# Kernel tuning notes

Measured on AMD Instinct MI355X. Metric: run time of the kernel, lower is better.

Reference implementation:

```python
import jax, jax.numpy as jnp
import numpy as np

D_MODEL = 1024
NUM_HEADS = 16
HEAD_DIM = D_MODEL // NUM_HEADS  # 64
# NOTE: the torch module passes scale=attention_head_size (NOT 1/sqrt(dh));
# we reproduce that exact math: scores are MULTIPLIED by head_dim.
SCALE = float(HEAD_DIM)

B, S = 2, 2048


def setup_inputs() -> dict:
    key = jax.random.key(0)
    ks = jax.random.split(key, 6)
    q = jax.random.normal(ks[0], (B, S, D_MODEL), dtype=jnp.float32)
    k = jax.random.normal(ks[1], (B, S, D_MODEL), dtype=jnp.float32)
    v = jax.random.normal(ks[2], (B, S, D_MODEL), dtype=jnp.float32)
    # Linear weights stored as [in, out]; scaled like typical init so the
    # (head_dim-scaled) logits stay numerically sane.
    w_std = 0.02
    Wq = jax.random.normal(ks[3], (D_MODEL, D_MODEL), dtype=jnp.float32) * w_std
    Wk = jax.random.normal(ks[4], (D_MODEL, D_MODEL), dtype=jnp.float32) * w_std
    Wv = jax.random.normal(ks[5], (D_MODEL, D_MODEL), dtype=jnp.float32) * w_std
    return {"q": q, "k": k, "v": v, "Wq": Wq, "Wk": Wk, "Wv": Wv}


def reference(q, k, v, Wq, Wk, Wv):
    Bq, Sq, _ = q.shape
    # QKV projections (qkv_bias=False), split into heads: [B, S, H, dh]
    qh = (q @ Wq).reshape(Bq, Sq, NUM_HEADS, HEAD_DIM)
    kh = (k @ Wk).reshape(Bq, Sq, NUM_HEADS, HEAD_DIM)
    vh = (v @ Wv).reshape(Bq, Sq, NUM_HEADS, HEAD_DIM)
    # Full materialized scores [B, H, Sq, Sk] -- the naive MHA pattern.
    sims = jnp.einsum("bqhd,bkhd->bhqk", qh, kh) * SCALE
    attn = jax.nn.softmax(sims, axis=-1)
    # Second matmul, then merge heads back: [B, S, D]
    out = jnp.einsum("bhqk,bkhd->bqhd", attn, vh).reshape(Bq, Sq, D_MODEL)
    return out
```

## Files before the change

kernel.cpp:

```cpp
#include <hip/hip_runtime.h>
#include <cstdint>
#include <cstddef>

typedef unsigned short u16;
typedef __bf16 bf16x8 __attribute__((ext_vector_type(8)));
typedef float f32x4 __attribute__((ext_vector_type(4)));
typedef unsigned int u32x4 __attribute__((ext_vector_type(4)));
typedef unsigned int u32x2 __attribute__((ext_vector_type(2)));
typedef u16 u16x4 __attribute__((ext_vector_type(4)));

typedef __attribute__((address_space(3))) void lds_void;
typedef __attribute__((address_space(1))) void glb_void;

constexpr float CEXP = 92.33248261689366f;

constexpr size_t XSZ = 4096ull * 1024ull;
constexpr size_t WSZ = 1024ull * 1024ull;
constexpr size_t OFF_XQH = 0;
constexpr size_t OFF_XQL = OFF_XQH + XSZ;
constexpr size_t OFF_XKH = OFF_XQL + XSZ;
constexpr size_t OFF_XKL = OFF_XKH + XSZ;
constexpr size_t OFF_XVH = OFF_XKL + XSZ;
constexpr size_t OFF_XVL = OFF_XVH + XSZ;
constexpr size_t OFF_WQH = OFF_XVL + XSZ;
constexpr size_t OFF_WQL = OFF_WQH + WSZ;
constexpr size_t OFF_WKH = OFF_WQL + WSZ;
constexpr size_t OFF_WKL = OFF_WKH + WSZ;
constexpr size_t OFF_WVH = OFF_WKL + WSZ;
constexpr size_t OFF_WVL = OFF_WVH + WSZ;
constexpr size_t OFF_QH  = OFF_WVL + WSZ;
constexpr size_t OFF_QL  = OFF_QH + XSZ;
constexpr size_t OFF_KH  = OFF_QL + XSZ;
constexpr size_t OFF_KL  = OFF_KH + XSZ;
constexpr size_t OFF_VH  = OFF_KL + XSZ;
constexpr size_t OFF_VT  = OFF_VH + XSZ;

__device__ __forceinline__ u16 f2b(float f) {
  unsigned u = __builtin_bit_cast(unsigned, f);
  return (u16)((u + 0x7FFFu + ((u >> 16) & 1u)) >> 16);
}
__device__ __forceinline__ float b2f(u16 h) {
  return __builtin_bit_cast(float, ((unsigned)h) << 16);
}
__device__ __forceinline__ bf16x8 ld8(const u16* p) {
  return __builtin_bit_cast(bf16x8, *(const u32x4*)p);
}
__device__ __forceinline__ unsigned pk2(float a, float b) {
#if __has_builtin(__builtin_amdgcn_cvt_pk_bf16_f32)
  auto v = __builtin_amdgcn_cvt_pk_bf16_f32(a, b);
  return __builtin_bit_cast(unsigned, v);
#else
  return (unsigned)f2b(a) | ((unsigned)f2b(b) << 16);
#endif
}
__device__ __forceinline__ float ex2(float x) {
#if __has_builtin(__builtin_amdgcn_exp2f)
  return __builtin_amdgcn_exp2f(x);
#else
  return exp2f(x);
#endif
}
__device__ __forceinline__ void glds16(const u16* g, u16* l) {
  __builtin_amdgcn_global_load_lds((const glb_void*)g, (lds_void*)l, 16, 0, 0);
}
__device__ __forceinline__ int swz32(int row, int cg) {
  return row * 32 + ((cg ^ ((row >> 1) & 3)) * 8);
}
__device__ __forceinline__ int swz64(int row, int cg) {
  return row * 64 + ((cg ^ (row & 7)) * 8);
}

__global__ __launch_bounds__(256) void convert_all(const float* __restrict__ q,
                                                   const float* __restrict__ k,
                                                   const float* __restrict__ v,
                                                   const float* __restrict__ Wq,
                                                   const float* __restrict__ Wk,
                                                   const float* __restrict__ Wv,
                                                   u16* __restrict__ ws) {
  __shared__ float tile[32][33];
  int id = blockIdx.x;
  int t = threadIdx.x;
  if (id < 12288) {
    int z = id >> 12, blk = id & 4095;
    const float* in = (z == 0) ? q : (z == 1) ? k : v;
    u16* hi = ws + ((z == 0) ? OFF_XQH : (z == 1) ? OFF_XKH : OFF_XVH);
    u16* lo = ws + ((z == 0) ? OFF_XQL : (z == 1) ? OFF_XKL : OFF_XVL);
    size_t i = ((size_t)blk * 256u + t) * 4u;
    float4 vv = *(const float4*)(in + i);
    float a[4] = {vv.x, vv.y, vv.z, vv.w};
    u16x4 hv, lv;
#pragma unroll
    for (int j = 0; j < 4; ++j) {
      u16 hb = f2b(a[j]);
      hv[j] = hb;
      lv[j] = f2b(a[j] - b2f(hb));
    }
    *(u16x4*)(hi + i) = hv;
    if (z != 2) *(u16x4*)(lo + i) = lv;
  } else {
    int r0 = id - 12288;
    int z = r0 >> 10, rem = r0 & 1023;
    const float* W = (z == 0) ? Wq : (z == 1) ? Wk : Wv;
    u16* hiT = ws + ((z == 0) ? OFF_WQH : (z == 1) ? OFF_WKH : OFF_WVH);
    u16* loT = ws + ((z == 0) ? OFF_WQL : (z == 1) ? OFF_WKL : OFF_WVL);
    int n0 = (rem & 31) * 32, k0 = (rem >> 5) * 32;
    int r = t >> 3, c0 = (t & 7) * 4;
    float4 vv = *(const float4*)(W + (size_t)(k0 + r) * 1024 + n0 + c0);
    tile[r][c0] = vv.x; tile[r][c0 + 1] = vv.y; tile[r][c0 + 2] = vv.z; tile[r][c0 + 3] = vv.w;
    __syncthreads();
    u16x4 hv, lv;
#pragma unroll
    for (int j = 0; j < 4; ++j) {
      float x = tile[c0 + j][r];
      u16 hb = f2b(x);
      hv[j] = hb;
      lv[j] = f2b(x - b2f(hb));
    }
    size_t o = (size_t)(n0 + r) * 1024 + k0 + c0;
    *(u16x4*)(hiT + o) = hv;
    if (z != 2) *(u16x4*)(loT + o) = lv;
  }
}

__global__ __launch_bounds__(256, 4) void gemm_qkv(u16* __restrict__ ws) {
  __shared__ u16 sA[2][64 * 32];
  __shared__ u16 sB[2][128 * 32];
  u16* cbuf = &sB[0][0];

  int id = blockIdx.x;
  int xcd = id & 7, seq = id >> 3;
  int pair = (seq >> 3) * 8 + xcd;
  int tile_n = seq & 7;
  int z = pair >> 6;
  int tile_m = pair & 63;

  const u16 *Ah, *Al, *Bh, *Bl; u16 *Oh, *Ol; bool split;
  if (z == 0)      { Ah = ws + OFF_XQH; Al = ws + OFF_XQL; Bh = ws + OFF_WQH; Bl = ws + OFF_WQL; Oh = ws + OFF_QH; Ol = ws + OFF_QL; split = true; }
  else if (z == 1) { Ah = ws + OFF_XKH; Al = ws + OFF_XKL; Bh = ws + OFF_WKH; Bl = ws + OFF_WKL; Oh = ws + OFF_KH; Ol = ws + OFF_KL; split = true; }
  else             { Ah = ws + OFF_XVH; Al = nullptr;      Bh = ws + OFF_WVH; Bl = nullptr;      Oh = ws + OFF_VT; Ol = nullptr;    split = false; }
  float oscale = (z == 0) ? CEXP : 1.0f;
  int m0 = tile_m * 64, n0 = tile_n * 128;
  int t = threadIdx.x, lane = t & 63, wave = t >> 6;
  int quad = lane >> 4, l15 = lane & 15;
  int wm = (wave >> 1) * 32, wn = (wave & 1) * 64;
  int rl = lane >> 2, cgl = lane & 3;
  f32x4 acc[2][4] = {};

  int rowA = wave * 16 + rl;
  size_t gA = (size_t)(m0 + rowA) * 1024 + (cgl ^ ((rowA >> 1) & 3)) * 8;
  int lbA = wave * 512;
  size_t gB[2]; int lbB[2];
#pragma unroll
  for (int i = 0; i < 2; ++i) {
    int rowB = wave * 32 + i * 16 + rl;
    gB[i] = (size_t)(n0 + rowB) * 1024 + (cgl ^ ((rowB >> 1) & 3)) * 8;
    lbB[i] = wave * 1024 + i * 512;
  }

  for (int kb = 0; kb < 32; ++kb) {
    int k0 = kb * 32;
    __syncthreads();
    glds16(Ah + gA + k0, &sA[0][lbA]);
    if (split) glds16(Al + gA + k0, &sA[1][lbA]);
#pragma unroll
    for (int i = 0; i < 2; ++i) {
      glds16(Bh + gB[i] + k0, &sB[0][lbB[i]]);
      if (split) glds16(Bl + gB[i] + k0, &sB[1][lbB[i]]);
    }
    __syncthreads();
    bf16x8 afh[2], afl[2], bfh[4], bfl[4];
#pragma unroll
    for (int mt = 0; mt < 2; ++mt) {
      int ra = wm + mt * 16 + l15;
      afh[mt] = ld8(&sA[0][swz32(ra, quad)]);
      if (split) afl[mt] = ld8(&sA[1][swz32(ra, quad)]);
    }
#pragma unroll
    for (int nt = 0; nt < 4; ++nt) {
      int rb = wn + nt * 16 + l15;
      bfh[nt] = ld8(&sB[0][swz32(rb, quad)]);
      if (split) bfl[nt] = ld8(&sB[1][swz32(rb, quad)]);
    }
#pragma unroll
    for (int mt = 0; mt < 2; ++mt)
#pragma unroll
      for (int nt = 0; nt < 4; ++nt) {
        acc[mt][nt] = __builtin_amdgcn_mfma_f32_16x16x32_bf16(afh[mt], bfh[nt], acc[mt][nt], 0, 0, 0);
        if (split) {
          acc[mt][nt] = __builtin_amdgcn_mfma_f32_16x16x32_bf16(afl[mt], bfh[nt], acc[mt][nt], 0, 0, 0);
          acc[mt][nt] = __builtin_amdgcn_mfma_f32_16x16x32_bf16(afh[mt], bfl[nt], acc[mt][nt], 0, 0, 0);
        }
      }
  }
  auto epi_round = [&](u16* dst, bool lo_round) {
#pragma unroll
    for (int mt = 0; mt < 2; ++mt)
#pragma unroll
      for (int nt = 0; nt < 4; ++nt)
#pragma unroll
        for (int r = 0; r < 4; ++r) {
          int row = wm + mt * 16 + quad * 4 + r;
          int col = wn + nt * 16 + l15;
          float v = acc[mt][nt][r] * oscale;
          u16 hb = f2b(v);
          u16 val = lo_round ? f2b(v - b2f(hb)) : hb;
          cbuf[row * 128 + (((col >> 3) ^ (row & 15)) * 8) + (col & 7)] = val;
        }
    __syncthreads();
    int row = t >> 2, seg = t & 3;
    int gm = m0 + row, bb = gm >> 11, s = gm & 2047;
    int hh = (n0 >> 6) + (seg >> 1), d0 = (seg & 1) * 32;
    u16* gp = dst + ((size_t)(bb * 16 + hh) * 2048 + s) * 64 + d0;
#pragma unroll
    for (int i = 0; i < 4; ++i) {
      int phys = (seg * 4 + i) ^ (row & 15);
      *(u32x4*)(gp + i * 8) = *(const u32x4*)(&cbuf[row * 128 + phys * 8]);
    }
  };
  __syncthreads();
  if (split) {
    epi_round(Oh, false);
    __syncthreads();
    epi_round(Ol, true);
  } else {
#pragma unroll
    for (int mt = 0; mt < 2; ++mt)
#pragma unroll
      for (int nt = 0; nt < 4; ++nt)
#pragma unroll
        for (int r = 0; r < 4; ++r) {
          int row = wm + mt * 16 + quad * 4 + r;
          int col = wn + nt * 16 + l15;
          cbuf[row * 128 + (((col >> 3) ^ (row & 15)) * 8) + (col & 7)] =
              f2b(acc[mt][nt][r]);
        }
    __syncthreads();
    int col = t >> 1, sh = t & 1;
    int hg = (n0 + col) >> 6, d = (n0 + col) & 63;
    int bb = m0 >> 11, s0 = m0 & 2047;
    u16 vals[32];
#pragma unroll
    for (int i = 0; i < 32; ++i) {
      int row = sh * 32 + i;
      vals[i] = cbuf[row * 128 + (((col >> 3) ^ (row & 15)) * 8) + (col & 7)];
    }
    u16* gp = Oh + ((size_t)((bb * 16 + hg) * 64 + d)) * 2048 + s0 + sh * 32;
#pragma unroll
    for (int i = 0; i < 4; ++i)
      *(u32x4*)(gp + i * 8) = *(const u32x4*)(&vals[i * 8]);
  }
}

__global__ __launch_bounds__(256, 4) void attn(const u16* __restrict__ ws,
                                               float* __restrict__ out) {
  __shared__ u16 lkh[64 * 64];
  __shared__ u16 lkl[64 * 64];
  __shared__ u16 lvt[64 * 64];
  __shared__ u16 lp[4][16 * 64];
  const u16* Qh = ws + OFF_QH; const u16* Ql = ws + OFF_QL;
  const u16* Kh = ws + OFF_KH; const u16* Kl = ws + OFF_KL;
  const u16* Vt = ws + OFF_VT;
  int b = blockIdx.z, h = blockIdx.y;
  int q0 = blockIdx.x * 64;
  int t = threadIdx.x, lane = t & 63, wave = t >> 6;
  int quad = lane >> 4, l15 = lane & 15;
  size_t hb = (size_t)(b * 16 + h) * (2048 * 64);
  bf16x8 onesf;
#pragma unroll
  for (int j = 0; j < 8; ++j) onesf[j] = __builtin_bit_cast(__bf16, (u16)0x3F80);
  int qrow = q0 + wave * 16 + l15;
  bf16x8 qfh[2], qfl[2];
#pragma unroll
  for (int ks = 0; ks < 2; ++ks) {
    size_t qo = hb + (size_t)qrow * 64 + ks * 32 + quad * 8;
    qfh[ks] = ld8(Qh + qo);
    qfl[ks] = ld8(Ql + qo);
  }
  float mi = -1e30f;
  f32x4 lsum = {};
  f32x4 o[4] = {};
  int rl = lane >> 3, cgl = lane & 7;

  size_t aK[2], aV[2]; int lb[2];
#pragma unroll
  for (int i = 0; i < 2; ++i) {
    int row = wave * 16 + i * 8 + rl;
    int cgg = cgl ^ (row & 7);
    aK[i] = hb + (size_t)row * 64 + cgg * 8;
    aV[i] = hb + (size_t)row * 2048 + cgg * 8;
    lb[i] = (wave * 16 + i * 8) * 64;
  }
  int soF[2][4];
#pragma unroll
  for (int ks = 0; ks < 2; ++ks)
#pragma unroll
    for (int nt = 0; nt < 4; ++nt)
      soF[ks][nt] = swz64(nt * 16 + l15, ks * 4 + quad);
  int soP[4];
  {
    int r7 = l15 & 7;
#pragma unroll
    for (int nt = 0; nt < 4; ++nt) {
      int c = nt * 2 + (quad >> 1);
      soP[nt] = l15 * 64 + ((c ^ r7) * 8) + (quad & 1) * 4;
    }
  }
  int soPa[2];
#pragma unroll
  for (int ks = 0; ks < 2; ++ks) soPa[ks] = swz64(l15, ks * 4 + quad);
  u16* lpw = &lp[wave][0];

#pragma unroll
  for (int i = 0; i < 2; ++i) {
    glds16(Kh + aK[i], &lkh[lb[i]]);
    glds16(Kl + aK[i], &lkl[lb[i]]);
    glds16(Vt + aV[i], &lvt[lb[i]]);
  }
  __syncthreads();

  for (int kt = 0; kt < 32; ++kt) {
    u32x4 pk_[2], pl_[2], pv_[2];
    if (kt < 31) {
#pragma unroll
      for (int i = 0; i < 2; ++i) {
        pk_[i] = *(const u32x4*)(Kh + aK[i] + (kt + 1) * 4096);
        pl_[i] = *(const u32x4*)(Kl + aK[i] + (kt + 1) * 4096);
        pv_[i] = *(const u32x4*)(Vt + aV[i] + (kt + 1) * 64);
      }
    }
    f32x4 sc[4] = {};
#pragma unroll
    for (int nt = 0; nt < 4; ++nt) {
#pragma unroll
      for (int ks = 0; ks < 2; ++ks) {
        bf16x8 kh_ = ld8(&lkh[soF[ks][nt]]);
        bf16x8 kl_ = ld8(&lkl[soF[ks][nt]]);
        sc[nt] = __builtin_amdgcn_mfma_f32_16x16x32_bf16(kh_, qfh[ks], sc[nt], 0, 0, 0);
        sc[nt] = __builtin_amdgcn_mfma_f32_16x16x32_bf16(kl_, qfh[ks], sc[nt], 0, 0, 0);
        sc[nt] = __builtin_amdgcn_mfma_f32_16x16x32_bf16(kh_, qfl[ks], sc[nt], 0, 0, 0);
      }
    }
    float mx = fmaxf(fmaxf(fmaxf(sc[0][0], sc[0][1]), fmaxf(sc[0][2], sc[0][3])),
                     fmaxf(fmaxf(sc[1][0], sc[1][1]), fmaxf(sc[1][2], sc[1][3])));
    float mx2 = fmaxf(fmaxf(fmaxf(sc[2][0], sc[2][1]), fmaxf(sc[2][2], sc[2][3])),
                      fmaxf(fmaxf(sc[3][0], sc[3][1]), fmaxf(sc[3][2], sc[3][3])));
    mx = fmaxf(mx, mx2);
    mx = fmaxf(mx, __shfl_xor(mx, 16));
    mx = fmaxf(mx, __shfl_xor(mx, 32));
    float mn = fmaxf(mi, mx);
    float alpha_s = ex2(mi - mn);
    mi = mn;
#pragma unroll
    for (int nt = 0; nt < 4; ++nt) {
      unsigned u01 = pk2(ex2(sc[nt][0] - mn), ex2(sc[nt][1] - mn));
      unsigned u23 = pk2(ex2(sc[nt][2] - mn), ex2(sc[nt][3] - mn));
      *(u32x2*)(&lpw[soP[nt]]) = u32x2{u01, u23};
    }
    float av[4];
#pragma unroll
    for (int r = 0; r < 4; ++r) av[r] = __shfl(alpha_s, quad * 4 + r);
#pragma unroll
    for (int r = 0; r < 4; ++r) {
      lsum[r] *= av[r];
      o[0][r] *= av[r]; o[1][r] *= av[r]; o[2][r] *= av[r]; o[3][r] *= av[r];
    }
    asm volatile("s_waitcnt lgkmcnt(0)" ::: "memory");
    bf16x8 pa[2];
#pragma unroll
    for (int ks = 0; ks < 2; ++ks) pa[ks] = ld8(&lpw[soPa[ks]]);
    lsum = __builtin_amdgcn_mfma_f32_16x16x32_bf16(pa[0], onesf, lsum, 0, 0, 0);
    lsum = __builtin_amdgcn_mfma_f32_16x16x32_bf16(pa[1], onesf, lsum, 0, 0, 0);
#pragma unroll
    for (int nt = 0; nt < 4; ++nt)
#pragma unroll
      for (int ks = 0; ks < 2; ++ks) {
        bf16x8 bv = ld8(&lvt[soF[ks][nt]]);
        o[nt] = __builtin_amdgcn_mfma_f32_16x16x32_bf16(pa[ks], bv, o[nt], 0, 0, 0);
      }
    __syncthreads();
    if (kt < 31) {
#pragma unroll
      for (int i = 0; i < 2; ++i) {
        *(u32x4*)(&lkh[lb[i] + lane * 8]) = pk_[i];
        *(u32x4*)(&lkl[lb[i] + lane * 8]) = pl_[i];
        *(u32x4*)(&lvt[lb[i] + lane * 8]) = pv_[i];
      }
    }
    __syncthreads();
  }
  float inv[4];
#pragma unroll
  for (int r = 0; r < 4; ++r) inv[r] = 1.0f / lsum[r];
#pragma unroll
  for (int nt = 0; nt < 4; ++nt)
#pragma unroll
    for (int r = 0; r < 4; ++r) {
      int srow = q0 + wave * 16 + quad * 4 + r;
      int d = nt * 16 + l15;
      out[(size_t)(b * 2048 + srow) * 1024 + h * 64 + d] = o[nt][r] * inv[r];
    }
}

extern "C" void kernel_launch(void* const* d_in, const int* in_sizes, int n_in,
                              void* d_out, int out_size, void* d_ws, size_t ws_size,
                              hipStream_t stream) {
  const float* q  = (const float*)d_in[0];
  const float* k  = (const float*)d_in[1];
  const float* v  = (const float*)d_in[2];
  const float* Wq = (const float*)d_in[3];
  const float* Wk = (const float*)d_in[4];
  const float* Wv = (const float*)d_in[5];
  u16* ws = (u16*)d_ws;
  float* out = (float*)d_out;

  convert_all<<<15360, 256, 0, stream>>>(q, k, v, Wq, Wk, Wv, ws);
  gemm_qkv<<<1536, 256, 0, stream>>>(ws);
  attn<<<dim3(32, 16, 2), 256, 0, stream>>>(ws, out);
}
```

Before: 278.7 us.

## Remap attention blocks per XCD, skip unneeded rescales, add MFMA priority hints

The attention grid becomes 1D and block ids are remapped so that each XCD handles four whole (batch, head) pairs. All query tiles that share K/V then hit the same L2. The online-softmax rescale of o and lsum is skipped when no row max in the wave grew, using a ballot. s_setprio raises wave priority around the MFMA sections, and the max reduction is rebalanced. Together these aim to cut L2 misses and VALU work, at the cost of a divergence check and a mapping that assumes exactly 1024 blocks and 8 XCDs.

```diff
diff --git a/kernel.cpp b/kernel.cpp
--- a/kernel.cpp
+++ b/kernel.cpp
@@ -260,11 +260,14 @@
   const u16* Qh = ws + OFF_QH; const u16* Ql = ws + OFF_QL;
   const u16* Kh = ws + OFF_KH; const u16* Kl = ws + OFF_KL;
   const u16* Vt = ws + OFF_VT;
-  int b = blockIdx.z, h = blockIdx.y;
-  int q0 = blockIdx.x * 64;
+  int id = blockIdx.x;
+  int xcd = id & 7, slot = id >> 3;
+  int hh = xcd * 4 + (slot >> 5);
+  int q0 = (slot & 31) * 64;
+  int b = hh >> 4, h = hh & 15;
   int t = threadIdx.x, lane = t & 63, wave = t >> 6;
   int quad = lane >> 4, l15 = lane & 15;
-  size_t hb = (size_t)(b * 16 + h) * (2048 * 64);
+  size_t hb = (size_t)hh * (2048 * 64);
   bf16x8 onesf;
 #pragma unroll
   for (int j = 0; j < 8; ++j) onesf[j] = __builtin_bit_cast(__bf16, (u16)0x3F80);
@@ -329,6 +332,7 @@
       }
     }
     f32x4 sc[4] = {};
+    __builtin_amdgcn_s_setprio(1);
 #pragma unroll
     for (int nt = 0; nt < 4; ++nt) {
 #pragma unroll
@@ -340,15 +344,18 @@
         sc[nt] = __builtin_amdgcn_mfma_f32_16x16x32_bf16(kh_, qfl[ks], sc[nt], 0, 0, 0);
       }
     }
-    float mx = fmaxf(fmaxf(fmaxf(sc[0][0], sc[0][1]), fmaxf(sc[0][2], sc[0][3])),
-                     fmaxf(fmaxf(sc[1][0], sc[1][1]), fmaxf(sc[1][2], sc[1][3])));
-    float mx2 = fmaxf(fmaxf(fmaxf(sc[2][0], sc[2][1]), fmaxf(sc[2][2], sc[2][3])),
-                      fmaxf(fmaxf(sc[3][0], sc[3][1]), fmaxf(sc[3][2], sc[3][3])));
-    mx = fmaxf(mx, mx2);
+    __builtin_amdgcn_s_setprio(0);
+    float t0 = fmaxf(fmaxf(sc[0][0], sc[0][1]), sc[0][2]);
+    float t1 = fmaxf(fmaxf(sc[0][3], sc[1][0]), sc[1][1]);
+    float t2 = fmaxf(fmaxf(sc[1][2], sc[1][3]), sc[2][0]);
+    float t3 = fmaxf(fmaxf(sc[2][1], sc[2][2]), sc[2][3]);
+    float t4 = fmaxf(fmaxf(sc[3][0], sc[3][1]), sc[3][2]);
+    float mx = fmaxf(fmaxf(fmaxf(t0, t1), fmaxf(t2, t3)), fmaxf(t4, sc[3][3]));
     mx = fmaxf(mx, __shfl_xor(mx, 16));
     mx = fmaxf(mx, __shfl_xor(mx, 32));
+    float mi_old = mi;
     float mn = fmaxf(mi, mx);
-    float alpha_s = ex2(mi - mn);
+    unsigned long long grew = __ballot(mx > mi);
     mi = mn;
 #pragma unroll
     for (int nt = 0; nt < 4; ++nt) {
@@ -356,18 +363,22 @@
       unsigned u23 = pk2(ex2(sc[nt][2] - mn), ex2(sc[nt][3] - mn));
       *(u32x2*)(&lpw[soP[nt]]) = u32x2{u01, u23};
     }
-    float av[4];
-#pragma unroll
-    for (int r = 0; r < 4; ++r) av[r] = __shfl(alpha_s, quad * 4 + r);
-#pragma unroll
-    for (int r = 0; r < 4; ++r) {
-      lsum[r] *= av[r];
-      o[0][r] *= av[r]; o[1][r] *= av[r]; o[2][r] *= av[r]; o[3][r] *= av[r];
+    if (grew) {
+      float alpha_s = ex2(mi_old - mn);
+      float av[4];
+#pragma unroll
+      for (int r = 0; r < 4; ++r) av[r] = __shfl(alpha_s, quad * 4 + r);
+#pragma unroll
+      for (int r = 0; r < 4; ++r) {
+        lsum[r] *= av[r];
+        o[0][r] *= av[r]; o[1][r] *= av[r]; o[2][r] *= av[r]; o[3][r] *= av[r];
+      }
     }
     asm volatile("s_waitcnt lgkmcnt(0)" ::: "memory");
     bf16x8 pa[2];
 #pragma unroll
     for (int ks = 0; ks < 2; ++ks) pa[ks] = ld8(&lpw[soPa[ks]]);
+    __builtin_amdgcn_s_setprio(1);
     lsum = __builtin_amdgcn_mfma_f32_16x16x32_bf16(pa[0], onesf, lsum, 0, 0, 0);
     lsum = __builtin_amdgcn_mfma_f32_16x16x32_bf16(pa[1], onesf, lsum, 0, 0, 0);
 #pragma unroll
@@ -377,6 +388,7 @@
         bf16x8 bv = ld8(&lvt[soF[ks][nt]]);
         o[nt] = __builtin_amdgcn_mfma_f32_16x16x32_bf16(pa[ks], bv, o[nt], 0, 0, 0);
       }
+    __builtin_amdgcn_s_setprio(0);
     __syncthreads();
     if (kt < 31) {
 #pragma unroll
@@ -415,5 +427,5 @@
 
   convert_all<<<15360, 256, 0, stream>>>(q, k, v, Wq, Wk, Wv, ws);
   gemm_qkv<<<1536, 256, 0, stream>>>(ws);
-  attn<<<dim3(32, 16, 2), 256, 0, stream>>>(ws, out);
-}
+  attn<<<1024, 256, 0, stream>>>(ws, out);
+}
```

Result: faster. 270.7 us (-2.9%).
